# Optimization experiments

Measured on AMD Instinct MI355X. Metric: run time of the kernel, lower is better.

The kernel has to match this reference:

```python
import jax, jax.numpy as jnp
import numpy as np

B, D = 8192, 1024
HR, HE, HF = 512, 4096, 2048
N_OPS, N_TASKS = 4, 4

def setup_inputs() -> dict:
    key = jax.random.key(0)
    ks = jax.random.split(key, 20)
    s = 0.02
    return {
        "x":        jax.random.normal(ks[0], (B, D), jnp.float32),
        # router
        "W_r1":   s*jax.random.normal(ks[1], (D, HR), jnp.float32),
        "b_r1":     jnp.zeros((HR,), jnp.float32),
        "W_dom":  s*jax.random.normal(ks[2], (HR, 2), jnp.float32),
        "b_dom":    jnp.zeros((2,), jnp.float32),
        "W_mop":  s*jax.random.normal(ks[3], (HR, N_OPS), jnp.float32),
        "W_lt":   s*jax.random.normal(ks[4], (HR, N_TASKS), jnp.float32),
        # math expert (operation hint = additive embedding)
        "op_emb": s*jax.random.normal(ks[5], (N_OPS, D), jnp.float32),
        "W_m1":   s*jax.random.normal(ks[6], (D, HE), jnp.float32),
        "b_m1":     jnp.zeros((HE,), jnp.float32),
        "W_m2":   s*jax.random.normal(ks[7], (HE, D), jnp.float32),
        "b_m2":     jnp.zeros((D,), jnp.float32),
        # language expert (task hint = additive embedding)
        "task_emb": s*jax.random.normal(ks[8], (N_TASKS, D), jnp.float32),
        "W_l1":   s*jax.random.normal(ks[9], (D, HE), jnp.float32),
        "b_l1":     jnp.zeros((HE,), jnp.float32),
        "W_l2":   s*jax.random.normal(ks[10], (HE, D), jnp.float32),
        "b_l2":     jnp.zeros((D,), jnp.float32),
        # fusion
        "W_f1":   s*jax.random.normal(ks[11], (D, HF), jnp.float32),
        "b_f1":     jnp.zeros((HF,), jnp.float32),
        "W_f2":   s*jax.random.normal(ks[12], (HF, D), jnp.float32),
        "b_f2":     jnp.zeros((D,), jnp.float32),
    }

def reference(x, W_r1, b_r1, W_dom, b_dom, W_mop, W_lt,
              op_emb, W_m1, b_m1, W_m2, b_m2,
              task_emb, W_l1, b_l1, W_l2, b_l2,
              W_f1, b_f1, W_f2, b_f2):
    # --- router ---
    h = jax.nn.relu(x @ W_r1 + b_r1)                      # [B, HR]
    dom_logits = h @ W_dom + b_dom                        # [B, 2]
    expert_weights = jax.nn.softmax(dom_logits, axis=-1)  # [B, 2]
    primary = jnp.argmax(dom_logits, axis=-1)             # [B]
    math_op = jnp.argmax(h @ W_mop, axis=-1)              # [B]
    lang_task = jnp.argmax(h @ W_lt, axis=-1)             # [B]
    # --- experts (vectorized equivalent of per-sample dispatch) ---
    math_in = x + op_emb[math_op]                         # [B, D]
    math_out = jax.nn.relu(math_in @ W_m1 + b_m1) @ W_m2 + b_m2
    lang_in = x + task_emb[lang_task]                     # [B, D]
    lang_out = jax.nn.relu(lang_in @ W_l1 + b_l1) @ W_l2 + b_l2
    selected = jnp.where((primary == 0)[:, None], math_out, lang_out)  # [B, D]
    # --- fusion: scale by routing weight of the chosen expert + MLP residual ---
    w = jnp.take_along_axis(expert_weights, primary[:, None], axis=1)  # [B, 1]
    fused = w * selected
    final = fused + jax.nn.relu(fused @ W_f1 + b_f1) @ W_f2 + b_f2     # [B, D]
    return final
```

## Files before the change

kernel.cpp:

```cpp
#include <hip/hip_runtime.h>
#include <hip/hip_bf16.h>
#include <stdint.h>

#define NB 8192
#define DD 1024
#define HRD 512
#define HED 4096
#define HFD 2048

typedef __attribute__((ext_vector_type(8))) short bf16x8;
typedef __attribute__((ext_vector_type(4))) float f32x4;
typedef unsigned short u16;

__device__ __forceinline__ u16 f2b(float f) {
    union { float f; uint32_t i; } c; c.f = f;
    uint32_t r = c.i + 0x7FFF + ((c.i >> 16) & 1);
    return (u16)(r >> 16);
}
__device__ __forceinline__ float b2f(u16 u) {
    union { uint32_t i; float f; } c; c.i = ((uint32_t)u) << 16; return c.f;
}

__device__ __forceinline__ void xcd_swz(int flat, int nwg, int nFast, int& f, int& s) {
    int xcd = flat & 7, rest = flat >> 3;
    int q = nwg >> 3, r = nwg & 7;
    int wg = (xcd < r ? xcd * (q + 1) : r * (q + 1) + (xcd - r) * q) + rest;
    f = wg % nFast; s = wg / nFast;
}

#define GLDS(g, l) __builtin_amdgcn_global_load_lds( \
    (const __attribute__((address_space(1))) void*)(g), \
    (__attribute__((address_space(3))) void*)(l), 16, 0, 0)

__global__ void k_init(int* cnt) { if (threadIdx.x < 2) cnt[threadIdx.x] = 0; }

__global__ __launch_bounds__(256) void k_split(const float4* __restrict__ x4,
                                               ushort4* __restrict__ hi4,
                                               ushort4* __restrict__ lo4) {
    int i = blockIdx.x * 256 + threadIdx.x;
    float4 v = x4[i];
    ushort4 h, l;
    h.x = f2b(v.x); l.x = f2b(v.x - b2f(h.x));
    h.y = f2b(v.y); l.y = f2b(v.y - b2f(h.y));
    h.z = f2b(v.z); l.z = f2b(v.z - b2f(h.z));
    h.w = f2b(v.w); l.w = f2b(v.w - b2f(h.w));
    hi4[i] = h; lo4[i] = l;
}

__global__ __launch_bounds__(256) void k_transpose(const float* __restrict__ in,
                                                   u16* __restrict__ out, int R, int C) {
    __shared__ float s[64][65];
    int tx = threadIdx.x & 63, ty = threadIdx.x >> 6;
    int c0 = blockIdx.x * 64, r0 = blockIdx.y * 64;
#pragma unroll
    for (int j = 0; j < 16; j++) { int r = ty + j * 4; s[r][tx] = in[(size_t)(r0 + r) * C + c0 + tx]; }
    __syncthreads();
#pragma unroll
    for (int j = 0; j < 16; j++) { int c = ty + j * 4; out[(size_t)(c0 + c) * R + r0 + tx] = f2b(s[tx][c]); }
}

__global__ __launch_bounds__(256) void k_transpose_split(const float* __restrict__ in,
                                                         u16* __restrict__ ohi, u16* __restrict__ olo,
                                                         int R, int C) {
    __shared__ float s[64][65];
    int tx = threadIdx.x & 63, ty = threadIdx.x >> 6;
    int c0 = blockIdx.x * 64, r0 = blockIdx.y * 64;
#pragma unroll
    for (int j = 0; j < 16; j++) { int r = ty + j * 4; s[r][tx] = in[(size_t)(r0 + r) * C + c0 + tx]; }
    __syncthreads();
#pragma unroll
    for (int j = 0; j < 16; j++) {
        int c = ty + j * 4;
        float v = s[tx][c];
        u16 h = f2b(v);
        ohi[(size_t)(c0 + c) * R + r0 + tx] = h;
        olo[(size_t)(c0 + c) * R + r0 + tx] = f2b(v - b2f(h));
    }
}

__device__ __forceinline__ void stage_tile(const char* gRowBase, long rowStrideBytes,
                                           u16* s, int tid) {
    int wave = tid >> 6, lane = tid & 63;
#pragma unroll
    for (int is = 0; is < 4; ++is) {
        int c = wave * 4 + is;
        int row = c * 8 + (lane >> 3);
        const char* g = gRowBase + (long)row * rowStrideBytes + (lane & 7) * 16;
        GLDS(g, (char*)s + c * 1024);
    }
}

__global__ __launch_bounds__(256) void k_router(const u16* __restrict__ Ah, const u16* __restrict__ Al,
                                                const u16* __restrict__ Bh, const u16* __restrict__ Bl,
                                                const float* __restrict__ bias, float* __restrict__ H) {
    __shared__ u16 sAh[2][128 * 64], sAl[2][128 * 64], sBh[2][128 * 64], sBl[2][128 * 64];
    int tid = threadIdx.x, lane = tid & 63, wave = tid >> 6;
    int flat = blockIdx.y * gridDim.x + blockIdx.x;
    int bm, bn;
    xcd_swz(flat, gridDim.x * gridDim.y, gridDim.y, bn, bm);
    f32x4 acc[4][4];
#pragma unroll
    for (int i = 0; i < 4; i++)
#pragma unroll
        for (int j = 0; j < 4; j++) acc[i][j] = (f32x4)0.f;
    int wm = (wave & 1) * 64, wn = (wave >> 1) * 64;
    const char* ahBase = (const char*)(Ah + (size_t)bm * 128 * DD);
    const char* alBase = (const char*)(Al + (size_t)bm * 128 * DD);
    const char* bhBase = (const char*)(Bh + (size_t)bn * 128 * DD);
    const char* blBase = (const char*)(Bl + (size_t)bn * 128 * DD);
    const int nk = DD / 64;
    stage_tile(ahBase, DD * 2, sAh[0], tid);
    stage_tile(alBase, DD * 2, sAl[0], tid);
    stage_tile(bhBase, DD * 2, sBh[0], tid);
    stage_tile(blBase, DD * 2, sBl[0], tid);
    asm volatile("s_waitcnt vmcnt(0)" ::: "memory");
    __builtin_amdgcn_s_barrier();
    int cur = 0;
    for (int it = 0; it < nk; ++it) {
        if (it + 1 < nk) {
            size_t ofs = (size_t)(it + 1) * 128;
            stage_tile(ahBase + ofs, DD * 2, sAh[cur ^ 1], tid);
            stage_tile(alBase + ofs, DD * 2, sAl[cur ^ 1], tid);
            stage_tile(bhBase + ofs, DD * 2, sBh[cur ^ 1], tid);
            stage_tile(blBase + ofs, DD * 2, sBl[cur ^ 1], tid);
        }
        const u16* pAh = sAh[cur]; const u16* pAl = sAl[cur];
        const u16* pBh = sBh[cur]; const u16* pBl = sBl[cur];
#pragma unroll
        for (int kk = 0; kk < 2; kk++) {
            int kofs = kk * 64 + (lane >> 4) * 16;
            bf16x8 vbh[4], vbl[4];
#pragma unroll
            for (int ni = 0; ni < 4; ni++) {
                int rB = (wn + ni * 16 + (lane & 15)) * 128 + kofs;
                vbh[ni] = *(const bf16x8*)((const char*)pBh + rB);
                vbl[ni] = *(const bf16x8*)((const char*)pBl + rB);
            }
#pragma unroll
            for (int mi = 0; mi < 4; mi++) {
                int rA = (wm + mi * 16 + (lane & 15)) * 128 + kofs;
                bf16x8 vah = *(const bf16x8*)((const char*)pAh + rA);
                bf16x8 val = *(const bf16x8*)((const char*)pAl + rA);
#pragma unroll
                for (int ni = 0; ni < 4; ni++) {
                    acc[mi][ni] = __builtin_amdgcn_mfma_f32_16x16x32_bf16(vah, vbh[ni], acc[mi][ni], 0, 0, 0);
                    acc[mi][ni] = __builtin_amdgcn_mfma_f32_16x16x32_bf16(vah, vbl[ni], acc[mi][ni], 0, 0, 0);
                    acc[mi][ni] = __builtin_amdgcn_mfma_f32_16x16x32_bf16(val, vbh[ni], acc[mi][ni], 0, 0, 0);
                }
            }
        }
        asm volatile("s_waitcnt vmcnt(0)" ::: "memory");
        __builtin_amdgcn_s_barrier();
        cur ^= 1;
    }
    int quad = lane >> 4, cl = lane & 15;
#pragma unroll
    for (int mi = 0; mi < 4; mi++)
#pragma unroll
        for (int r = 0; r < 4; r++) {
            int row = bm * 128 + wm + mi * 16 + quad * 4 + r;
#pragma unroll
            for (int ni = 0; ni < 4; ni++) {
                int col = bn * 128 + wn + ni * 16 + cl;
                float v = acc[mi][ni][r] + bias[col];
                H[(size_t)row * HRD + col] = fmaxf(v, 0.f);
            }
        }
}

__global__ __launch_bounds__(256) void k_heads(const float* __restrict__ H,
                                               const float* __restrict__ Wd, const float* __restrict__ bd,
                                               const float* __restrict__ Wm, const float* __restrict__ Wl,
                                               int* __restrict__ cnt, int* __restrict__ perm,
                                               float* __restrict__ wsc, int* __restrict__ eic) {
    int lane = threadIdx.x & 63, wave = threadIdx.x >> 6;
    int r = blockIdx.x * 4 + wave;
    const float4* h4 = (const float4*)(H + (size_t)r * HRD);
    float4 v0 = h4[lane * 2], v1 = h4[lane * 2 + 1];
    float hv[8] = {v0.x, v0.y, v0.z, v0.w, v1.x, v1.y, v1.z, v1.w};
    float a[10];
#pragma unroll
    for (int t = 0; t < 10; t++) a[t] = 0.f;
    int kbase = lane * 8;
#pragma unroll
    for (int j = 0; j < 8; j++) {
        int k = kbase + j;
        float h_ = hv[j];
        float2 wd = ((const float2*)Wd)[k];
        a[0] += h_ * wd.x; a[1] += h_ * wd.y;
        float4 wm = ((const float4*)Wm)[k];
        a[2] += h_ * wm.x; a[3] += h_ * wm.y; a[4] += h_ * wm.z; a[5] += h_ * wm.w;
        float4 wl = ((const float4*)Wl)[k];
        a[6] += h_ * wl.x; a[7] += h_ * wl.y; a[8] += h_ * wl.z; a[9] += h_ * wl.w;
    }
#pragma unroll
    for (int t = 0; t < 10; t++)
#pragma unroll
        for (int off = 32; off > 0; off >>= 1) a[t] += __shfl_down(a[t], off);
    if (lane == 0) {
        float d0 = a[0] + bd[0], d1 = a[1] + bd[1];
        int primary = (d1 > d0) ? 1 : 0;
        float w = 1.f / (1.f + expf(-fabsf(d0 - d1)));
        int mi = 0; float mv = a[2];
        if (a[3] > mv) { mv = a[3]; mi = 1; }
        if (a[4] > mv) { mv = a[4]; mi = 2; }
        if (a[5] > mv) { mv = a[5]; mi = 3; }
        int li = 0; float lv = a[6];
        if (a[7] > lv) { lv = a[7]; li = 1; }
        if (a[8] > lv) { lv = a[8]; li = 2; }
        int pos;
        if (a[9] > lv) { lv = a[9]; li = 3; }
        if (primary == 0) pos = atomicAdd(&cnt[0], 1);
        else              pos = NB - 1 - atomicAdd(&cnt[1], 1);
        perm[pos] = r; wsc[pos] = w; eic[pos] = (primary == 0) ? mi : li;
    }
}

__global__ __launch_bounds__(256) void k_gather(const float* __restrict__ x,
                                                const float* __restrict__ op_emb,
                                                const float* __restrict__ task_emb,
                                                const int* __restrict__ perm, const int* __restrict__ eic,
                                                const int* __restrict__ cnt, u16* __restrict__ xin) {
    int lane = threadIdx.x & 63, wave = threadIdx.x >> 6;
    int i = blockIdx.x * 4 + wave;
    int n0 = cnt[0];
    int r = perm[i];
    const float* emb = ((i >= n0) ? task_emb : op_emb) + (size_t)eic[i] * DD;
    const float4* x4 = (const float4*)(x + (size_t)r * DD);
    const float4* e4 = (const float4*)emb;
    ushort4* o4 = (ushort4*)(xin + (size_t)i * DD);
#pragma unroll
    for (int j = 0; j < 4; j++) {
        int idx = lane + j * 64;
        float4 xv = x4[idx], ev = e4[idx];
        ushort4 o;
        o.x = f2b(xv.x + ev.x); o.y = f2b(xv.y + ev.y);
        o.z = f2b(xv.z + ev.z); o.w = f2b(xv.w + ev.w);
        o4[idx] = o;
    }
}

template <bool DUAL>
__global__ __launch_bounds__(512) void k_g256(
    const u16* __restrict__ A, const u16* __restrict__ B0w, const u16* __restrict__ B1w,
    const float* __restrict__ bias0, const float* __restrict__ bias1,
    u16* __restrict__ Out, int K, int N, const int* __restrict__ cnt) {
    __shared__ __align__(16) u16 sA[2][256 * 64];
    __shared__ __align__(16) u16 sB[2][256 * 64];
    const int tid = threadIdx.x, lane = tid & 63, wave = tid >> 6;
    int flat = blockIdx.y * gridDim.x + blockIdx.x;
    int t, bn;
    xcd_swz(flat, gridDim.x * gridDim.y, gridDim.y, bn, t);

    int tile = t, storeLo = 0, storeHi = 0x7fffffff;
    const u16* Bt = B0w; const float* bias = bias0;
    if constexpr (DUAL) {
        int n0 = cnt[0];
        int tb = n0 >> 8;
        bool isMath = (t <= tb) && (t < NB / 256);
        tile = isMath ? t : (t - 1);
        if (isMath) { storeLo = tile * 256; storeHi = n0 < storeLo + 256 ? n0 : storeLo + 256; }
        else        { storeHi = tile * 256 + 256; storeLo = n0 > tile * 256 ? n0 : tile * 256;
                      Bt = B1w; bias = bias1; }
        if (storeLo >= storeHi) return;
    }

    f32x4 acc[8][4];
#pragma unroll
    for (int i = 0; i < 8; i++)
#pragma unroll
        for (int j = 0; j < 4; j++) acc[i][j] = (f32x4)0.f;

    const int wm = (wave & 1) * 128;
    const int wn = (wave >> 1) * 64;
    const int rl = lane & 15, q = lane >> 4, x7 = lane & 7;

    const long stride = (long)K * 2;
    const char* aBase = (const char*)A + (size_t)tile * 256 * stride;
    const char* bBase = (const char*)Bt + (size_t)bn * 256 * stride;
    const int rowInUnit = tid >> 3;
    const long srcOfs = (long)((tid & 7) ^ (rowInUnit & 7)) << 4;
    const int waveOfs = wave * 1024;

    auto SH = [&](const char* gBase, u16* ldsArr, int h, int kt) {
        long kofs = (long)kt * 128 + srcOfs;
#pragma unroll
        for (int i = 0; i < 2; i++)
            GLDS(gBase + (long)(h * 128 + i * 64 + rowInUnit) * stride + kofs,
                 (char*)ldsArr + h * 16384 + i * 8192 + waveOfs);
    };
    auto STAGEF = [&](int kt, int d) {
        SH(aBase, sA[d], 0, kt); SH(aBase, sA[d], 1, kt);
        SH(bBase, sB[d], 0, kt); SH(bBase, sB[d], 1, kt);
    };

    const int nk = K >> 6;
    STAGEF(0, 0);
    bf16x8 va[4][2], vb0[2][2], vb1[2][2];
    for (int kt = 0; kt < nk; ++kt) {
        const int cur = kt & 1;
        if (kt + 1 < nk) {
            STAGEF(kt + 1, cur ^ 1);
            asm volatile("s_waitcnt vmcnt(8)" ::: "memory");
        } else {
            asm volatile("s_waitcnt vmcnt(0)" ::: "memory");
        }
        __builtin_amdgcn_s_barrier();
        const char* pA = (const char*)&sA[cur][0];
        const char* pB = (const char*)&sB[cur][0];
#pragma unroll
        for (int f = 0; f < 4; f++)
#pragma unroll
            for (int kk = 0; kk < 2; kk++)
                va[f][kk] = *(const bf16x8*)(pA + (wm + f * 16 + rl) * 128 + (((kk * 4 + q) ^ x7) << 4));
#pragma unroll
        for (int g = 0; g < 2; g++)
#pragma unroll
            for (int kk = 0; kk < 2; kk++)
                vb0[g][kk] = *(const bf16x8*)(pB + (wn + g * 16 + rl) * 128 + (((kk * 4 + q) ^ x7) << 4));
        __builtin_amdgcn_s_setprio(1);
#pragma unroll
        for (int f = 0; f < 4; f++)
#pragma unroll
            for (int g = 0; g < 2; g++)
#pragma unroll
                for (int kk = 0; kk < 2; kk++)
                    acc[f][g] = __builtin_amdgcn_mfma_f32_16x16x32_bf16(va[f][kk], vb0[g][kk], acc[f][g], 0, 0, 0);
        __builtin_amdgcn_s_setprio(0);
#pragma unroll
        for (int g = 0; g < 2; g++)
#pragma unroll
            for (int kk = 0; kk < 2; kk++)
                vb1[g][kk] = *(const bf16x8*)(pB + (wn + 32 + g * 16 + rl) * 128 + (((kk * 4 + q) ^ x7) << 4));
        __builtin_amdgcn_s_setprio(1);
#pragma unroll
        for (int f = 0; f < 4; f++)
#pragma unroll
            for (int g = 0; g < 2; g++)
#pragma unroll
                for (int kk = 0; kk < 2; kk++)
                    acc[f][2 + g] = __builtin_amdgcn_mfma_f32_16x16x32_bf16(va[f][kk], vb1[g][kk], acc[f][2 + g], 0, 0, 0);
        __builtin_amdgcn_s_setprio(0);
#pragma unroll
        for (int f = 0; f < 4; f++)
#pragma unroll
            for (int kk = 0; kk < 2; kk++)
                va[f][kk] = *(const bf16x8*)(pA + (wm + 64 + f * 16 + rl) * 128 + (((kk * 4 + q) ^ x7) << 4));
        __builtin_amdgcn_s_setprio(1);
#pragma unroll
        for (int f = 0; f < 4; f++)
#pragma unroll
            for (int g = 0; g < 2; g++)
#pragma unroll
                for (int kk = 0; kk < 2; kk++)
                    acc[4 + f][2 + g] = __builtin_amdgcn_mfma_f32_16x16x32_bf16(va[f][kk], vb1[g][kk], acc[4 + f][2 + g], 0, 0, 0);
        __builtin_amdgcn_s_setprio(0);
        __builtin_amdgcn_s_setprio(1);
#pragma unroll
        for (int f = 0; f < 4; f++)
#pragma unroll
            for (int g = 0; g < 2; g++)
#pragma unroll
                for (int kk = 0; kk < 2; kk++)
                    acc[4 + f][g] = __builtin_amdgcn_mfma_f32_16x16x32_bf16(va[f][kk], vb0[g][kk], acc[4 + f][g], 0, 0, 0);
        __builtin_amdgcn_s_setprio(0);
        asm volatile("" ::: "memory");
        __builtin_amdgcn_s_barrier();
    }

    const int quad = lane >> 4, cl = lane & 15;
#pragma unroll
    for (int f = 0; f < 8; f++)
#pragma unroll
        for (int rr = 0; rr < 4; rr++) {
            int grow = tile * 256 + wm + f * 16 + quad * 4 + rr;
            if constexpr (DUAL) { if (grow < storeLo || grow >= storeHi) continue; }
#pragma unroll
            for (int g = 0; g < 4; g++) {
                int col = bn * 256 + wn + g * 16 + cl;
                float v = acc[f][g][rr] + bias[col];
                Out[(size_t)grow * N + col] = f2b(fmaxf(v, 0.f));
            }
        }
}

template <int EPI, bool DUAL>
__global__ __launch_bounds__(512) void k_gemm8p(
    const u16* __restrict__ A, const u16* __restrict__ B0, const u16* __restrict__ B1,
    const float* __restrict__ bias0, const float* __restrict__ bias1,
    void* __restrict__ Out, int K, int N,
    const int* __restrict__ cnt, const float* __restrict__ wsel,
    const int* __restrict__ perm, const u16* __restrict__ resid) {
    __shared__ __align__(16) u16 sA[2][128 * 64];
    __shared__ __align__(16) u16 sB[2][128 * 64];
    const int tid = threadIdx.x, lane = tid & 63, wave = tid >> 6;
    int flat = blockIdx.y * gridDim.x + blockIdx.x;
    int t, bn;
    xcd_swz(flat, gridDim.x * gridDim.y, gridDim.y, bn, t);

    int n0 = 0, tile = t, storeLo = 0, storeHi = 0x7fffffff;
    const u16* Bt = B0; const float* bias = bias0;
    if constexpr (DUAL) {
        n0 = cnt[0];
        int tb = n0 >> 7;
        bool isMath = (t <= tb) && (t < 64);
        tile = isMath ? t : (t - 1);
        if (isMath) { storeLo = tile * 128; storeHi = n0 < storeLo + 128 ? n0 : storeLo + 128; }
        else        { storeHi = tile * 128 + 128; storeLo = n0 > tile * 128 ? n0 : tile * 128;
                      Bt = B1; bias = bias1; }
        if (storeLo >= storeHi) return;
    }

    f32x4 acc[4][2];
#pragma unroll
    for (int i = 0; i < 4; i++)
#pragma unroll
        for (int j = 0; j < 2; j++) acc[i][j] = (f32x4)0.f;

    const int wm = (wave & 1) * 64;
    const int wn = (wave >> 1) * 32;
    const int rl = lane & 15, q = lane >> 4, x7 = lane & 7;

    const long stride = (long)K * 2;
    const char* aBase = (const char*)A + (size_t)tile * 128 * stride;
    const char* bBase = (const char*)Bt + (size_t)bn * 128 * stride;
    const int rowInUnit = tid >> 3;
    const long srcOfs = (long)((tid & 7) ^ (rowInUnit & 7)) << 4;
    const int ldsWaveOfs = wave * 1024;

    auto STAGE = [&](int kt, int d) {
        long kofs = (long)kt * 128 + srcOfs;
#pragma unroll
        for (int i = 0; i < 2; i++)
            GLDS(aBase + (long)(i * 64 + rowInUnit) * stride + kofs,
                 (char*)&sA[d][0] + i * 8192 + ldsWaveOfs);
#pragma unroll
        for (int i = 0; i < 2; i++)
            GLDS(bBase + (long)(i * 64 + rowInUnit) * stride + kofs,
                 (char*)&sB[d][0] + i * 8192 + ldsWaveOfs);
    };

    STAGE(0, 0);
    const int nk = K >> 6;
    for (int k = 0; k < nk; ++k) {
        const int r_ = k & 1;
        if (k + 1 < nk) {
            STAGE(k + 1, r_ ^ 1);
            asm volatile("s_waitcnt vmcnt(4)" ::: "memory");
        } else {
            asm volatile("s_waitcnt vmcnt(0)" ::: "memory");
        }
        __builtin_amdgcn_s_barrier();
        const char* pA = (const char*)&sA[r_][0];
        const char* pB = (const char*)&sB[r_][0];
        bf16x8 vaA[2][2], vaB[2][2], vb0[2], vb1[2];
#pragma unroll
        for (int f = 0; f < 2; f++)
#pragma unroll
            for (int kk = 0; kk < 2; kk++)
                vaA[f][kk] = *(const bf16x8*)(pA + (wm + f * 16 + rl) * 128 + (((kk * 4 + q) ^ x7) << 4));
#pragma unroll
        for (int kk = 0; kk < 2; kk++)
            vb0[kk] = *(const bf16x8*)(pB + (wn + rl) * 128 + (((kk * 4 + q) ^ x7) << 4));
        __builtin_amdgcn_s_setprio(1);
#pragma unroll
        for (int f = 0; f < 2; f++)
#pragma unroll
            for (int kk = 0; kk < 2; kk++)
                acc[f][0] = __builtin_amdgcn_mfma_f32_16x16x32_bf16(vaA[f][kk], vb0[kk], acc[f][0], 0, 0, 0);
        __builtin_amdgcn_s_setprio(0);
#pragma unroll
        for (int kk = 0; kk < 2; kk++)
            vb1[kk] = *(const bf16x8*)(pB + (wn + 16 + rl) * 128 + (((kk * 4 + q) ^ x7) << 4));
        __builtin_amdgcn_s_setprio(1);
#pragma unroll
        for (int f = 0; f < 2; f++)
#pragma unroll
            for (int kk = 0; kk < 2; kk++)
                acc[f][1] = __builtin_amdgcn_mfma_f32_16x16x32_bf16(vaA[f][kk], vb1[kk], acc[f][1], 0, 0, 0);
        __builtin_amdgcn_s_setprio(0);
#pragma unroll
        for (int f = 0; f < 2; f++)
#pragma unroll
            for (int kk = 0; kk < 2; kk++)
                vaB[f][kk] = *(const bf16x8*)(pA + (wm + 32 + f * 16 + rl) * 128 + (((kk * 4 + q) ^ x7) << 4));
        __builtin_amdgcn_s_setprio(1);
#pragma unroll
        for (int f = 0; f < 2; f++)
#pragma unroll
            for (int kk = 0; kk < 2; kk++)
                acc[2 + f][1] = __builtin_amdgcn_mfma_f32_16x16x32_bf16(vaB[f][kk], vb1[kk], acc[2 + f][1], 0, 0, 0);
        __builtin_amdgcn_s_setprio(0);
        __builtin_amdgcn_s_setprio(1);
#pragma unroll
        for (int f = 0; f < 2; f++)
#pragma unroll
            for (int kk = 0; kk < 2; kk++)
                acc[2 + f][0] = __builtin_amdgcn_mfma_f32_16x16x32_bf16(vaB[f][kk], vb0[kk], acc[2 + f][0], 0, 0, 0);
        __builtin_amdgcn_s_setprio(0);
        asm volatile("" ::: "memory");
        __builtin_amdgcn_s_barrier();
    }

    const int quad = lane >> 4, cl = lane & 15;
#pragma unroll
    for (int mi = 0; mi < 4; mi++)
#pragma unroll
        for (int r = 0; r < 4; r++) {
            int grow = tile * 128 + wm + mi * 16 + quad * 4 + r;
            if constexpr (DUAL) { if (grow < storeLo || grow >= storeHi) continue; }
#pragma unroll
            for (int ni = 0; ni < 2; ni++) {
                int col = bn * 128 + wn + ni * 16 + cl;
                float v = acc[mi][ni][r] + bias[col];
                if constexpr (EPI == 0) {
                    ((u16*)Out)[(size_t)grow * N + col] = f2b(fmaxf(v, 0.f));
                } else if constexpr (EPI == 1) {
                    ((u16*)Out)[(size_t)grow * N + col] = f2b(v * wsel[grow]);
                } else {
                    v += b2f(resid[(size_t)grow * N + col]);
                    ((float*)Out)[(size_t)perm[grow] * N + col] = v;
                }
            }
        }
}

extern "C" void kernel_launch(void* const* d_in, const int* in_sizes, int n_in,
                              void* d_out, int out_size, void* d_ws, size_t ws_size,
                              hipStream_t stream) {
    const float* x      = (const float*)d_in[0];
    const float* W_r1   = (const float*)d_in[1];
    const float* b_r1   = (const float*)d_in[2];
    const float* W_dom  = (const float*)d_in[3];
    const float* b_dom  = (const float*)d_in[4];
    const float* W_mop  = (const float*)d_in[5];
    const float* W_lt   = (const float*)d_in[6];
    const float* op_emb = (const float*)d_in[7];
    const float* W_m1   = (const float*)d_in[8];
    const float* b_m1   = (const float*)d_in[9];
    const float* W_m2   = (const float*)d_in[10];
    const float* b_m2   = (const float*)d_in[11];
    const float* task_emb = (const float*)d_in[12];
    const float* W_l1   = (const float*)d_in[13];
    const float* b_l1   = (const float*)d_in[14];
    const float* W_l2   = (const float*)d_in[15];
    const float* b_l2   = (const float*)d_in[16];
    const float* W_f1   = (const float*)d_in[17];
    const float* b_f1   = (const float*)d_in[18];
    const float* W_f2   = (const float*)d_in[19];
    const float* b_f2   = (const float*)d_in[20];

    char* wsp = (char*)d_ws;
    size_t off = 0;
    auto take = [&](size_t bytes) -> char* {
        char* p = wsp + off;
        off += (bytes + 255) & ~(size_t)255;
        return p;
    };
    u16* Wr_hi = (u16*)take((size_t)HRD * DD * 2);
    u16* Wr_lo = (u16*)take((size_t)HRD * DD * 2);
    u16* Wm1t  = (u16*)take((size_t)HED * DD * 2);
    u16* Wl1t  = (u16*)take((size_t)HED * DD * 2);
    u16* Wm2t  = (u16*)take((size_t)DD * HED * 2);
    u16* Wl2t  = (u16*)take((size_t)DD * HED * 2);
    u16* Wf1t  = (u16*)take((size_t)HFD * DD * 2);
    u16* Wf2t  = (u16*)take((size_t)DD * HFD * 2);
    u16* x_hi  = (u16*)take((size_t)NB * DD * 2);
    u16* x_lo  = (u16*)take((size_t)NB * DD * 2);
    float* Hbuf = (float*)take((size_t)NB * HRD * 4);
    u16* hid   = (u16*)take((size_t)NB * HED * 2);
    int* cnt   = (int*)take(256);
    int* perm  = (int*)take(NB * 4);
    int* eic   = (int*)take(NB * 4);
    float* wsc = (float*)take(NB * 4);
    u16* xin   = x_hi;
    u16* fused = x_lo;
    u16* hid2  = Wm1t;

    k_init<<<1, 64, 0, stream>>>(cnt);
    k_split<<<(NB * DD / 4) / 256, 256, 0, stream>>>((const float4*)x, (ushort4*)x_hi, (ushort4*)x_lo);
    k_transpose_split<<<dim3(HRD / 64, DD / 64), 256, 0, stream>>>(W_r1, Wr_hi, Wr_lo, DD, HRD);
    k_transpose<<<dim3(HED / 64, DD / 64), 256, 0, stream>>>(W_m1, Wm1t, DD, HED);
    k_transpose<<<dim3(HED / 64, DD / 64), 256, 0, stream>>>(W_l1, Wl1t, DD, HED);
    k_transpose<<<dim3(DD / 64, HED / 64), 256, 0, stream>>>(W_m2, Wm2t, HED, DD);
    k_transpose<<<dim3(DD / 64, HED / 64), 256, 0, stream>>>(W_l2, Wl2t, HED, DD);
    k_transpose<<<dim3(HFD / 64, DD / 64), 256, 0, stream>>>(W_f1, Wf1t, DD, HFD);
    k_transpose<<<dim3(DD / 64, HFD / 64), 256, 0, stream>>>(W_f2, Wf2t, HFD, DD);

    k_router<<<dim3(NB / 128, HRD / 128), 256, 0, stream>>>(x_hi, x_lo, Wr_hi, Wr_lo, b_r1, Hbuf);
    k_heads<<<NB / 4, 256, 0, stream>>>(Hbuf, W_dom, b_dom, W_mop, W_lt, cnt, perm, wsc, eic);
    k_gather<<<NB / 4, 256, 0, stream>>>(x, op_emb, task_emb, perm, eic, cnt, xin);

    k_g256<true><<<dim3(NB / 256 + 1, HED / 256), 512, 0, stream>>>(
        xin, Wm1t, Wl1t, b_m1, b_l1, hid, DD, HED, cnt);
    k_gemm8p<1, true><<<dim3(NB / 128 + 1, DD / 128), 512, 0, stream>>>(
        hid, Wm2t, Wl2t, b_m2, b_l2, fused, HED, DD, cnt, wsc, nullptr, nullptr);
    k_g256<false><<<dim3(NB / 256, HFD / 256), 512, 0, stream>>>(
        fused, Wf1t, nullptr, b_f1, nullptr, hid2, DD, HFD, cnt);
    k_gemm8p<2, false><<<dim3(NB / 128, DD / 128), 512, 0, stream>>>(
        hid2, Wf2t, nullptr, b_f2, nullptr, d_out, HFD, DD, cnt, nullptr, perm, fused);
}
```

Before: 679.9 us.

## Stage GEMM operand loads per quadrant with finer-grained prefetch interleaving

Reworks the 256x256 GEMM main loop so A and B halves are loaded into LDS in separate quarter-stages, each issued right after the LDS reads of the buffer region it will overwrite. Global-to-LDS copies are spread across the four MFMA phases of each k-step, with barriers between phases and a two-iterations-ahead prefetch for parts of the tiles. The LDS row mapping and epilogue row/column indexing are permuted to match. The aim is better overlap of memory traffic with MFMA work, at the cost of more barriers per iteration and more complex buffer-reuse ordering.

Result: faster. 647.6 us (-4.8%).

```diff
diff --git a/kernel.cpp b/kernel.cpp
--- a/kernel.cpp
+++ b/kernel.cpp
@@ -274,87 +274,113 @@
     const int wm = (wave & 1) * 128;
     const int wn = (wave >> 1) * 64;
     const int rl = lane & 15, q = lane >> 4, x7 = lane & 7;
+    const int aRow = (wave & 1) * 64;
+    const int bRow = (wave >> 1) * 32;
 
     const long stride = (long)K * 2;
     const char* aBase = (const char*)A + (size_t)tile * 256 * stride;
     const char* bBase = (const char*)Bt + (size_t)bn * 256 * stride;
-    const int rowInUnit = tid >> 3;
-    const long srcOfs = (long)((tid & 7) ^ (rowInUnit & 7)) << 4;
+    const long srcOfs = (long)((lane & 7) ^ (lane >> 3)) << 4;
     const int waveOfs = wave * 1024;
-
-    auto SH = [&](const char* gBase, u16* ldsArr, int h, int kt) {
+    const int l8 = lane >> 3;
+
+    auto SH_A = [&](int h, int kt, int d) {
         long kofs = (long)kt * 128 + srcOfs;
 #pragma unroll
-        for (int i = 0; i < 2; i++)
-            GLDS(gBase + (long)(h * 128 + i * 64 + rowInUnit) * stride + kofs,
-                 (char*)ldsArr + h * 16384 + i * 8192 + waveOfs);
+        for (int i = 0; i < 2; i++) {
+            int gr = wave * 8 + l8 + h * 64 + i * 128;
+            GLDS(aBase + (long)gr * stride + kofs,
+                 (char*)&sA[d][0] + h * 16384 + i * 8192 + waveOfs);
+        }
     };
-    auto STAGEF = [&](int kt, int d) {
-        SH(aBase, sA[d], 0, kt); SH(aBase, sA[d], 1, kt);
-        SH(bBase, sB[d], 0, kt); SH(bBase, sB[d], 1, kt);
+    auto SH_B = [&](int h, int kt, int d) {
+        long kofs = (long)kt * 128 + srcOfs;
+#pragma unroll
+        for (int i = 0; i < 2; i++) {
+            int rp = i * 64 + wave * 8 + l8;
+            int gn = (rp & 31) + ((rp >> 5) << 6) + h * 32;
+            GLDS(bBase + (long)gn * stride + kofs,
+                 (char*)&sB[d][0] + h * 16384 + i * 8192 + waveOfs);
+        }
     };
 
     const int nk = K >> 6;
-    STAGEF(0, 0);
+    SH_A(0, 0, 0); SH_B(0, 0, 0); SH_B(1, 0, 0); SH_A(1, 0, 0);
+    if (nk > 1) {
+        SH_A(0, 1, 1); SH_B(0, 1, 1); SH_B(1, 1, 1);
+        asm volatile("s_waitcnt vmcnt(6)" ::: "memory");
+    } else {
+        asm volatile("s_waitcnt vmcnt(0)" ::: "memory");
+    }
+    __builtin_amdgcn_s_barrier();
+
     bf16x8 va[4][2], vb0[2][2], vb1[2][2];
     for (int kt = 0; kt < nk; ++kt) {
         const int cur = kt & 1;
-        if (kt + 1 < nk) {
-            STAGEF(kt + 1, cur ^ 1);
-            asm volatile("s_waitcnt vmcnt(8)" ::: "memory");
+        const char* pA = (const char*)&sA[cur][0];
+        const char* pB = (const char*)&sB[cur][0];
+#pragma unroll
+        for (int f = 0; f < 4; f++)
+#pragma unroll
+            for (int kk = 0; kk < 2; kk++)
+                va[f][kk] = *(const bf16x8*)(pA + (aRow + f * 16 + rl) * 128 + (((kk * 4 + q) ^ x7) << 4));
+#pragma unroll
+        for (int g = 0; g < 2; g++)
+#pragma unroll
+            for (int kk = 0; kk < 2; kk++)
+                vb0[g][kk] = *(const bf16x8*)(pB + (bRow + g * 16 + rl) * 128 + (((kk * 4 + q) ^ x7) << 4));
+        if (kt + 1 < nk) SH_A(1, kt + 1, cur ^ 1);
+        __builtin_amdgcn_s_setprio(1);
+#pragma unroll
+        for (int f = 0; f < 4; f++)
+#pragma unroll
+            for (int g = 0; g < 2; g++)
+#pragma unroll
+                for (int kk = 0; kk < 2; kk++)
+                    acc[f][g] = __builtin_amdgcn_mfma_f32_16x16x32_bf16(va[f][kk], vb0[g][kk], acc[f][g], 0, 0, 0);
+        __builtin_amdgcn_s_setprio(0);
+        asm volatile("" ::: "memory");
+        __builtin_amdgcn_s_barrier();
+#pragma unroll
+        for (int g = 0; g < 2; g++)
+#pragma unroll
+            for (int kk = 0; kk < 2; kk++)
+                vb1[g][kk] = *(const bf16x8*)(pB + (bRow + 128 + g * 16 + rl) * 128 + (((kk * 4 + q) ^ x7) << 4));
+        if (kt + 2 < nk) SH_B(0, kt + 2, cur);
+        __builtin_amdgcn_s_setprio(1);
+#pragma unroll
+        for (int f = 0; f < 4; f++)
+#pragma unroll
+            for (int g = 0; g < 2; g++)
+#pragma unroll
+                for (int kk = 0; kk < 2; kk++)
+                    acc[f][2 + g] = __builtin_amdgcn_mfma_f32_16x16x32_bf16(va[f][kk], vb1[g][kk], acc[f][2 + g], 0, 0, 0);
+        __builtin_amdgcn_s_setprio(0);
+        asm volatile("" ::: "memory");
+        __builtin_amdgcn_s_barrier();
+#pragma unroll
+        for (int f = 0; f < 4; f++)
+#pragma unroll
+            for (int kk = 0; kk < 2; kk++)
+                va[f][kk] = *(const bf16x8*)(pA + (aRow + 128 + f * 16 + rl) * 128 + (((kk * 4 + q) ^ x7) << 4));
+        if (kt + 2 < nk) SH_B(1, kt + 2, cur);
+        __builtin_amdgcn_s_setprio(1);
+#pragma unroll
+        for (int f = 0; f < 4; f++)
+#pragma unroll
+            for (int g = 0; g < 2; g++)
+#pragma unroll
+                for (int kk = 0; kk < 2; kk++)
+                    acc[4 + f][2 + g] = __builtin_amdgcn_mfma_f32_16x16x32_bf16(va[f][kk], vb1[g][kk], acc[4 + f][2 + g], 0, 0, 0);
+        __builtin_amdgcn_s_setprio(0);
+        asm volatile("" ::: "memory");
+        __builtin_amdgcn_s_barrier();
+        if (kt + 2 < nk) {
+            SH_A(0, kt + 2, cur);
+            asm volatile("s_waitcnt vmcnt(6)" ::: "memory");
         } else {
             asm volatile("s_waitcnt vmcnt(0)" ::: "memory");
         }
-        __builtin_amdgcn_s_barrier();
-        const char* pA = (const char*)&sA[cur][0];
-        const char* pB = (const char*)&sB[cur][0];
-#pragma unroll
-        for (int f = 0; f < 4; f++)
-#pragma unroll
-            for (int kk = 0; kk < 2; kk++)
-                va[f][kk] = *(const bf16x8*)(pA + (wm + f * 16 + rl) * 128 + (((kk * 4 + q) ^ x7) << 4));
-#pragma unroll
-        for (int g = 0; g < 2; g++)
-#pragma unroll
-            for (int kk = 0; kk < 2; kk++)
-                vb0[g][kk] = *(const bf16x8*)(pB + (wn + g * 16 + rl) * 128 + (((kk * 4 + q) ^ x7) << 4));
-        __builtin_amdgcn_s_setprio(1);
-#pragma unroll
-        for (int f = 0; f < 4; f++)
-#pragma unroll
-            for (int g = 0; g < 2; g++)
-#pragma unroll
-                for (int kk = 0; kk < 2; kk++)
-                    acc[f][g] = __builtin_amdgcn_mfma_f32_16x16x32_bf16(va[f][kk], vb0[g][kk], acc[f][g], 0, 0, 0);
-        __builtin_amdgcn_s_setprio(0);
-#pragma unroll
-        for (int g = 0; g < 2; g++)
-#pragma unroll
-            for (int kk = 0; kk < 2; kk++)
-                vb1[g][kk] = *(const bf16x8*)(pB + (wn + 32 + g * 16 + rl) * 128 + (((kk * 4 + q) ^ x7) << 4));
-        __builtin_amdgcn_s_setprio(1);
-#pragma unroll
-        for (int f = 0; f < 4; f++)
-#pragma unroll
-            for (int g = 0; g < 2; g++)
-#pragma unroll
-                for (int kk = 0; kk < 2; kk++)
-                    acc[f][2 + g] = __builtin_amdgcn_mfma_f32_16x16x32_bf16(va[f][kk], vb1[g][kk], acc[f][2 + g], 0, 0, 0);
-        __builtin_amdgcn_s_setprio(0);
-#pragma unroll
-        for (int f = 0; f < 4; f++)
-#pragma unroll
-            for (int kk = 0; kk < 2; kk++)
-                va[f][kk] = *(const bf16x8*)(pA + (wm + 64 + f * 16 + rl) * 128 + (((kk * 4 + q) ^ x7) << 4));
-        __builtin_amdgcn_s_setprio(1);
-#pragma unroll
-        for (int f = 0; f < 4; f++)
-#pragma unroll
-            for (int g = 0; g < 2; g++)
-#pragma unroll
-                for (int kk = 0; kk < 2; kk++)
-                    acc[4 + f][2 + g] = __builtin_amdgcn_mfma_f32_16x16x32_bf16(va[f][kk], vb1[g][kk], acc[4 + f][2 + g], 0, 0, 0);
-        __builtin_amdgcn_s_setprio(0);
         __builtin_amdgcn_s_setprio(1);
 #pragma unroll
         for (int f = 0; f < 4; f++)
@@ -373,11 +399,11 @@
     for (int f = 0; f < 8; f++)
 #pragma unroll
         for (int rr = 0; rr < 4; rr++) {
-            int grow = tile * 256 + wm + f * 16 + quad * 4 + rr;
+            int grow = tile * 256 + wm + ((f & 3) * 16) + ((f >> 2) * 64) + quad * 4 + rr;
             if constexpr (DUAL) { if (grow < storeLo || grow >= storeHi) continue; }
 #pragma unroll
             for (int g = 0; g < 4; g++) {
-                int col = bn * 256 + wn + g * 16 + cl;
+                int col = bn * 256 + wn + ((g & 1) * 16) + ((g >> 1) * 32) + cl;
                 float v = acc[f][g][rr] + bias[col];
                 Out[(size_t)grow * N + col] = f2b(fmaxf(v, 0.f));
             }
```
